# Performance work log

Hardware: AMD Instinct MI355X
Metric: run time of the kernel (lower is better)

Reference implementation:

```python
import jax, jax.numpy as jnp
import numpy as np

B, L, DIM = 4, 2048, 512
H, D = 8, 64
SCALE = D ** -0.5
NEG = -10000.0


def setup_inputs() -> dict:
    key = jax.random.key(0)
    ks = jax.random.split(key, 5)
    std = 1.0 / np.sqrt(DIM)
    return {
        "x": jax.random.normal(ks[0], (B, L, DIM), dtype=jnp.float32),
        "wq": jax.random.normal(ks[1], (H * D, DIM), dtype=jnp.float32) * std,
        "wk": jax.random.normal(ks[2], (H * D, DIM), dtype=jnp.float32) * std,
        "wv": jax.random.normal(ks[3], (H * D, DIM), dtype=jnp.float32) * std,
        "wo": jax.random.normal(ks[4], (DIM, H * D), dtype=jnp.float32) * std,
    }


def reference(x, wq, wk, wv, wo):
    b, l, _ = x.shape
    # projections (torch Linear: y = x @ W.T), split heads -> [b,h,l,d]
    q = (x @ wq.T).reshape(b, l, H, D).transpose(0, 2, 1, 3)
    k = (x @ wk.T).reshape(b, l, H, D).transpose(0, 2, 1, 3)
    v = (x @ wv.T).reshape(b, l, H, D).transpose(0, 2, 1, 3)
    scores = jnp.einsum("bhld,bhsd->bhls", q, k) * SCALE
    scores = jnp.nan_to_num(scores, nan=0.0, posinf=10000.0, neginf=NEG)
    diag = jnp.eye(l, dtype=bool)[None, None]  # [1,1,l,l]
    scores = jnp.where(diag, NEG, scores)
    attn = jax.nn.softmax(scores, axis=-1)
    attn = jnp.where(diag, 0.0, attn)
    attn = jnp.nan_to_num(attn, nan=0.0, posinf=0.0, neginf=0.0)
    out = jnp.einsum("bhls,bhsd->bhld", attn, v)
    out = out.transpose(0, 2, 1, 3).reshape(b, l, H * D)
    return out @ wo.T
```

## Files before the change

### kernel.cpp

```cpp
#include <hip/hip_runtime.h>
#include <hip/hip_bf16.h>


#define Bsz 4
#define Lsz 2048
#define DIMsz 512
#define Hsz 8
#define Dsz 64

typedef _Float16 f16;
typedef __attribute__((ext_vector_type(8))) _Float16 f16x8;
typedef __attribute__((ext_vector_type(4))) _Float16 f16x4;
typedef __attribute__((ext_vector_type(2))) __fp16 fp16x2;
typedef __attribute__((ext_vector_type(4))) float f32x4;
typedef __attribute__((ext_vector_type(16))) float f32x16;
typedef unsigned int u32;
typedef __attribute__((ext_vector_type(2))) unsigned int u32x2;

#if __has_builtin(__builtin_amdgcn_exp2f)
#define EXP2(x) __builtin_amdgcn_exp2f(x)
#else
#define EXP2(x) __expf(0.6931471805599453f * (x))
#endif

__device__ __forceinline__ u32 pack2(float a, float b) {
#if __has_builtin(__builtin_amdgcn_cvt_pkrtz)
    fp16x2 h = __builtin_amdgcn_cvt_pkrtz(a, b);
    return __builtin_bit_cast(u32, h);
#else
    fp16x2 h; h.x = (__fp16)a; h.y = (__fp16)b;
    return __builtin_bit_cast(u32, h);
#endif
}

__device__ __forceinline__ float addpair(u32 p, float c) {
#if __has_builtin(__builtin_amdgcn_fdot2)
    fp16x2 ones; ones.x = (__fp16)1.0f; ones.y = (__fp16)1.0f;
    return __builtin_amdgcn_fdot2(__builtin_bit_cast(fp16x2, p), ones, c, false);
#else
    fp16x2 h = __builtin_bit_cast(fp16x2, p);
    return c + (float)h.x + (float)h.y;
#endif
}

#if __has_builtin(__builtin_amdgcn_permlane32_swap)
__device__ __forceinline__ void plswap(u32& a, u32& b) {
    u32x2 r = __builtin_amdgcn_permlane32_swap(a, b, false, false);
    a = r.x; b = r.y;
}
#else
__device__ __forceinline__ void plswap(u32& a, u32& b) {
    u32 sa = (u32)__shfl_xor((int)a, 32);
    u32 sb = (u32)__shfl_xor((int)b, 32);
    bool hi = (threadIdx.x & 32) != 0;
    u32 na = hi ? sb : a;
    u32 nb = hi ? b : sa;
    a = na; b = nb;
}
#endif

__device__ __forceinline__ void gl2lds16(const void* g, void* l) {
    __builtin_amdgcn_global_load_lds(
        (const __attribute__((address_space(1))) u32*)g,
        (__attribute__((address_space(3))) u32*)l, 16, 0, 0);
}

__global__ __launch_bounds__(256) void pack_f16(
    const float* __restrict__ x, const float* __restrict__ wq,
    const float* __restrict__ wk, const float* __restrict__ wv,
    const float* __restrict__ wo,
    f16* __restrict__ xh, f16* __restrict__ w3h, f16* __restrict__ woh)
{
    int bx = blockIdx.x, seg, blk;
    if (bx < 4096) { seg = 0; blk = bx; }
    else { seg = 1 + ((bx - 4096) >> 8); blk = (bx - 4096) & 255; }
    const float* s; f16* d; float sc = 1.0f;
    switch (seg) {
        case 0: s = x;  d = xh;            break;
        case 1: s = wq; d = w3h;           sc = 0.18033688011112042f; break;
        case 2: s = wk; d = w3h + 262144;  break;
        case 3: s = wv; d = w3h + 524288;  break;
        default: s = wo; d = woh;          break;
    }
    int i = (blk * 256 + threadIdx.x) * 4;
    float4 v = *(const float4*)(s + i);
    f16x4 o;
    o.x = (f16)(v.x * sc); o.y = (f16)(v.y * sc);
    o.z = (f16)(v.z * sc); o.w = (f16)(v.w * sc);
    *(f16x4*)(d + i) = o;
}

__global__ __launch_bounds__(256) void gemm_qkv_f16(
    const f16* __restrict__ A, const f16* __restrict__ B,
    f16* __restrict__ qh, f16* __restrict__ kh, f16* __restrict__ vth)
{
    __shared__ __align__(16) char smem[32768];
    f16* Ash = (f16*)smem;
    f16* Bsh = (f16*)(smem + 16384);

    const int tid = threadIdx.x;
    const int w = tid >> 6, lane = tid & 63;
    const int quad = lane >> 4, low = lane & 15;
    const int wm = w >> 1, wn = w & 1;
    const int m0 = blockIdx.y * 128, n0 = blockIdx.x * 128;

    f32x4 acc[4][4];
    #pragma unroll
    for (int i = 0; i < 4; i++)
        #pragma unroll
        for (int j = 0; j < 4; j++) acc[i][j] = (f32x4){0.f, 0.f, 0.f, 0.f};

    #pragma unroll 1
    for (int k0 = 0; k0 < DIMsz; k0 += 64) {
        __syncthreads();
        #pragma unroll
        for (int j = 0; j < 4; j++) {
            int t = j * 256 + tid;
            int r = t >> 3, g = t & 7;
            int gc = (g ^ (r & 7)) * 8;
            char* lb = (char*)Ash + (j * 256 + w * 64) * 16;
            gl2lds16(A + (size_t)(m0 + r) * DIMsz + k0 + gc, lb);
            char* lb2 = (char*)Bsh + (j * 256 + w * 64) * 16;
            gl2lds16(B + (size_t)(n0 + r) * DIMsz + k0 + gc, lb2);
        }
        __syncthreads();

        #pragma unroll
        for (int ks2 = 0; ks2 < 2; ks2++) {
            f16x8 af[4], bf[4];
            #pragma unroll
            for (int mt = 0; mt < 4; mt++) {
                int ar = wm * 64 + mt * 16 + low;
                int c = ks2 * 4 + quad;
                af[mt] = *(const f16x8*)&Ash[ar * 64 + ((c ^ (ar & 7)) << 3)];
            }
            #pragma unroll
            for (int nt = 0; nt < 4; nt++) {
                int br = wn * 64 + nt * 16 + low;
                int c = ks2 * 4 + quad;
                bf[nt] = *(const f16x8*)&Bsh[br * 64 + ((c ^ (br & 7)) << 3)];
            }
            #pragma unroll
            for (int mt = 0; mt < 4; mt++)
                #pragma unroll
                for (int nt = 0; nt < 4; nt++)
                    acc[mt][nt] = __builtin_amdgcn_mfma_f32_16x16x32_f16(
                        af[mt], bf[nt], acc[mt][nt], 0, 0, 0);
        }
    }

    const int proj = n0 >> 9;
    if (proj < 2) {
        f16* dst = (proj == 0) ? qh : kh;
        #pragma unroll
        for (int nt = 0; nt < 4; nt++) {
            int n = n0 + wn * 64 + nt * 16 + low;
            int c = n & 511, h = c >> 6, d = c & 63;
            #pragma unroll
            for (int mt = 0; mt < 4; mt++)
                #pragma unroll
                for (int r = 0; r < 4; r++) {
                    int m = m0 + wm * 64 + mt * 16 + quad * 4 + r;
                    int b_ = m >> 11, l = m & (Lsz - 1);
                    size_t bh = (size_t)(b_ * Hsz + h);
                    dst[(bh * Lsz + l) * Dsz + d] = (f16)acc[mt][nt][r];
                }
        }
    } else {
        const int hb = (n0 & 511) >> 6;
        f16* Tv = (f16*)smem;
        const int b_ = m0 >> 11, l0 = m0 & (Lsz - 1);
        #pragma unroll 1
        for (int hs = 0; hs < 2; hs++) {
            __syncthreads();
            if (wn == hs) {
                #pragma unroll
                for (int nt = 0; nt < 4; nt++) {
                    int d = nt * 16 + low;
                    #pragma unroll
                    for (int mt = 0; mt < 4; mt++)
                        #pragma unroll
                        for (int r = 0; r < 4; r++) {
                            int l = wm * 64 + mt * 16 + quad * 4 + r;
                            Tv[d * 136 + l] = (f16)acc[mt][nt][r];
                        }
                }
            }
            __syncthreads();
            int d = tid >> 2, seg = tid & 3;
            size_t bh = (size_t)(b_ * Hsz + hb + hs);
            f16* dstp = vth + (bh * 64 + d) * (size_t)Lsz + l0 + seg * 32;
            const f16* srcp = Tv + d * 136 + seg * 32;
            #pragma unroll
            for (int j = 0; j < 4; j++)
                *(f16x8*)(dstp + j * 8) = *(const f16x8*)(srcp + j * 8);
        }
    }
}

__global__ __launch_bounds__(256, 2) void attn_mfma(
    const f16* __restrict__ q, const f16* __restrict__ k,
    const f16* __restrict__ vt, f16* __restrict__ ctx)
{
    __shared__ __align__(16) char smem[65536];
    __shared__ float Ls[4][2][32];

    const int tid = threadIdx.x;
    const int w = tid >> 6, lane = tid & 63;
    const int col = lane & 31;
    const int h = lane >> 5;
    const int bh = blockIdx.x;
    const int qb = blockIdx.y;
    const int q0 = qb * 64;
    const size_t kvb = (size_t)bh * Lsz;

    f16x8 qf[2][4];
    #pragma unroll
    for (int qt = 0; qt < 2; qt++)
        #pragma unroll
        for (int s = 0; s < 4; s++)
            qf[qt][s] = *(const f16x8*)(q + (kvb + q0 + qt * 32 + col) * Dsz
                                          + s * 16 + h * 8);

    const f16* kp; const f16* vp;
    {
        int rk = tid >> 3, gk = tid & 7;
        kp = k + (kvb + rk) * Dsz + ((gk ^ (rk & 7)) << 3);
        int rv = tid >> 4, gv = tid & 15;
        vp = vt + ((size_t)bh * Dsz + rv) * Lsz + ((gv ^ (rv & 15)) << 3);
    }

    char* kl[2]; char* vl[2];
    const f16* kfp[2][4];
    const f16* vfp[2][2][2];
    const int rk = w * 32 + col;
    #pragma unroll
    for (int b = 0; b < 2; b++) {
        f16* Ks = (f16*)(smem + b * 32768);
        f16* Vs = (f16*)(smem + b * 32768 + 16384);
        kl[b] = (char*)Ks + (w * 64) * 16;
        vl[b] = (char*)Vs + (w * 64) * 16;
        #pragma unroll
        for (int s = 0; s < 4; s++)
            kfp[b][s] = Ks + rk * 64 + (((s * 2 + h) ^ (rk & 7)) << 3);
        #pragma unroll
        for (int dt = 0; dt < 2; dt++)
            #pragma unroll
            for (int ks = 0; ks < 2; ks++) {
                int rv = dt * 32 + col, cv = w * 4 + ks * 2 + h;
                vfp[b][dt][ks] = Vs + rv * 128 + ((cv ^ (rv & 15)) << 3);
            }
    }

    f32x16 acc[2][2];
    #pragma unroll
    for (int qt = 0; qt < 2; qt++)
        #pragma unroll
        for (int dt = 0; dt < 2; dt++)
            #pragma unroll
            for (int i = 0; i < 16; i++) acc[qt][dt][i] = 0.f;
    float lsum[2] = {0.f, 0.f};

    const int drnd_i = qb >> 1;
    const int dqt = w - (qb & 1) * 2;

    gl2lds16(kp,        kl[0]);
    gl2lds16(kp + 2048, kl[0] + 4096);
    gl2lds16(kp + 4096, kl[0] + 8192);
    gl2lds16(kp + 6144, kl[0] + 12288);
    gl2lds16(vp,            vl[0]);
    gl2lds16(vp + 16 * Lsz, vl[0] + 4096);
    gl2lds16(vp + 32 * Lsz, vl[0] + 8192);
    gl2lds16(vp + 48 * Lsz, vl[0] + 12288);
    kp += 128 * Dsz; vp += 128;
    __syncthreads();

    int b = 0;
    #pragma unroll 1
    for (int r = 0; r < 16; r++) {
        if (r < 15) {
            char* knl = kl[b ^ 1]; char* vnl = vl[b ^ 1];
            gl2lds16(kp,        knl);
            gl2lds16(kp + 2048, knl + 4096);
            gl2lds16(kp + 4096, knl + 8192);
            gl2lds16(kp + 6144, knl + 12288);
            gl2lds16(vp,            vnl);
            gl2lds16(vp + 16 * Lsz, vnl + 4096);
            gl2lds16(vp + 32 * Lsz, vnl + 8192);
            gl2lds16(vp + 48 * Lsz, vnl + 12288);
            kp += 128 * Dsz; vp += 128;
        }

        f32x16 st[2];
        #pragma unroll
        for (int i = 0; i < 16; i++) { st[0][i] = 0.f; st[1][i] = 0.f; }
        #pragma unroll
        for (int s = 0; s < 4; s++) {
            f16x8 kf = *(const f16x8*)kfp[b][s];
            st[0] = __builtin_amdgcn_mfma_f32_32x32x16_f16(kf, qf[0][s], st[0], 0, 0, 0);
            st[1] = __builtin_amdgcn_mfma_f32_32x32x16_f16(kf, qf[1][s], st[1], 0, 0, 0);
        }

        union { u32 u[4]; f16x8 v; } pf[2][2];
        const bool drnd = (r == drnd_i);
        #pragma unroll
        for (int qt = 0; qt < 2; qt++) {
            float pv[16];
            #pragma unroll
            for (int i = 0; i < 16; i++) pv[i] = EXP2(st[qt][i]);
            if (drnd && qt == dqt) {
                #pragma unroll
                for (int i = 0; i < 16; i++) {
                    int row = (i & 3) + 8 * (i >> 2) + 4 * h;
                    pv[i] = (row == col) ? 0.f : pv[i];
                }
            }
            u32 P2[8];
            #pragma unroll
            for (int j = 0; j < 8; j++) {
                P2[j] = pack2(pv[2 * j], pv[2 * j + 1]);
                lsum[qt] = addpair(P2[j], lsum[qt]);
            }
            plswap(P2[0], P2[2]); plswap(P2[1], P2[3]);
            plswap(P2[4], P2[6]); plswap(P2[5], P2[7]);
            #pragma unroll
            for (int jj = 0; jj < 4; jj++) {
                pf[qt][0].u[jj] = P2[jj];
                pf[qt][1].u[jj] = P2[4 + jj];
            }
        }

        #pragma unroll
        for (int dt = 0; dt < 2; dt++)
            #pragma unroll
            for (int ks = 0; ks < 2; ks++) {
                f16x8 vf = *(const f16x8*)vfp[b][dt][ks];
                acc[0][dt] = __builtin_amdgcn_mfma_f32_32x32x16_f16(
                    vf, pf[0][ks].v, acc[0][dt], 0, 0, 0);
                acc[1][dt] = __builtin_amdgcn_mfma_f32_32x32x16_f16(
                    vf, pf[1][ks].v, acc[1][dt], 0, 0, 0);
            }

        __syncthreads();
        b ^= 1;
    }

    #pragma unroll
    for (int qt = 0; qt < 2; qt++) {
        lsum[qt] += __shfl_xor(lsum[qt], 32);
        if (h == 0) Ls[w][qt][col] = lsum[qt];
    }

    float* Om = (float*)smem;
    __syncthreads();
    if (w == 1 || w == 3) {
        float* og = Om + (w >> 1) * 4096;
        #pragma unroll
        for (int qt = 0; qt < 2; qt++)
            #pragma unroll
            for (int dt = 0; dt < 2; dt++)
                #pragma unroll
                for (int i = 0; i < 16; i++) {
                    int row = (i & 3) + 8 * (i >> 2) + 4 * h;
                    og[(dt * 32 + row) * 64 + qt * 32 + col] = acc[qt][dt][i];
                }
    }
    __syncthreads();
    if (w == 0 || w == 2) {
        const float* og = Om + (w >> 1) * 4096;
        #pragma unroll
        for (int qt = 0; qt < 2; qt++)
            #pragma unroll
            for (int dt = 0; dt < 2; dt++)
                #pragma unroll
                for (int i = 0; i < 16; i++) {
                    int row = (i & 3) + 8 * (i >> 2) + 4 * h;
                    acc[qt][dt][i] += og[(dt * 32 + row) * 64 + qt * 32 + col];
                }
    }
    __syncthreads();
    if (w == 2) {
        #pragma unroll
        for (int qt = 0; qt < 2; qt++)
            #pragma unroll
            for (int dt = 0; dt < 2; dt++)
                #pragma unroll
                for (int i = 0; i < 16; i++) {
                    int row = (i & 3) + 8 * (i >> 2) + 4 * h;
                    Om[(dt * 32 + row) * 64 + qt * 32 + col] = acc[qt][dt][i];
                }
    }
    __syncthreads();
    if (w == 0) {
        #pragma unroll
        for (int qt = 0; qt < 2; qt++)
            #pragma unroll
            for (int dt = 0; dt < 2; dt++)
                #pragma unroll
                for (int i = 0; i < 16; i++) {
                    int row = (i & 3) + 8 * (i >> 2) + 4 * h;
                    acc[qt][dt][i] += Om[(dt * 32 + row) * 64 + qt * 32 + col];
                }
        const int bb = bh >> 3, hh = bh & 7;
        #pragma unroll
        for (int qt = 0; qt < 2; qt++) {
            float ls = Ls[0][qt][col] + Ls[1][qt][col]
                     + Ls[2][qt][col] + Ls[3][qt][col];
            const float inv = 1.0f / ls;
            f16* op = ctx + ((size_t)(bb * Lsz + q0 + qt * 32 + col)) * DIMsz
                          + hh * 64;
            #pragma unroll
            for (int dt = 0; dt < 2; dt++)
                #pragma unroll
                for (int r4 = 0; r4 < 4; r4++) {
                    f16x4 o;
                    o.x = (f16)(acc[qt][dt][4 * r4 + 0] * inv);
                    o.y = (f16)(acc[qt][dt][4 * r4 + 1] * inv);
                    o.z = (f16)(acc[qt][dt][4 * r4 + 2] * inv);
                    o.w = (f16)(acc[qt][dt][4 * r4 + 3] * inv);
                    *(f16x4*)(op + dt * 32 + 8 * r4 + 4 * h) = o;
                }
        }
    }
}

__global__ __launch_bounds__(256) void gemm_out_f16(
    const f16* __restrict__ A, const f16* __restrict__ B,
    float* __restrict__ C)
{
    __shared__ f16 Ash[64 * 64];
    __shared__ f16 Bsh[64 * 64];
    const int tid = threadIdx.x;
    const int w = tid >> 6, lane = tid & 63;
    const int quad = lane >> 4, low = lane & 15;
    const int wm = w >> 1, wn = w & 1;
    const int m0 = blockIdx.y * 64, n0 = blockIdx.x * 64;

    f32x4 acc[2][2];
    #pragma unroll
    for (int i = 0; i < 2; i++)
        #pragma unroll
        for (int j = 0; j < 2; j++) acc[i][j] = (f32x4){0.f, 0.f, 0.f, 0.f};

    #pragma unroll 1
    for (int k0 = 0; k0 < DIMsz; k0 += 64) {
        __syncthreads();
        #pragma unroll
        for (int j = 0; j < 2; j++) {
            int t = j * 256 + tid;
            int r = t >> 3, g = t & 7;
            int gc = (g ^ (r & 7)) * 8;
            char* lb = (char*)Ash + (j * 256 + w * 64) * 16;
            gl2lds16(A + (size_t)(m0 + r) * DIMsz + k0 + gc, lb);
            char* lb2 = (char*)Bsh + (j * 256 + w * 64) * 16;
            gl2lds16(B + (size_t)(n0 + r) * DIMsz + k0 + gc, lb2);
        }
        __syncthreads();

        #pragma unroll
        for (int ks2 = 0; ks2 < 2; ks2++) {
            f16x8 af[2], bf[2];
            #pragma unroll
            for (int mt = 0; mt < 2; mt++) {
                int ar = wm * 32 + mt * 16 + low;
                int c = ks2 * 4 + quad;
                af[mt] = *(const f16x8*)&Ash[ar * 64 + ((c ^ (ar & 7)) << 3)];
            }
            #pragma unroll
            for (int nt = 0; nt < 2; nt++) {
                int br = wn * 32 + nt * 16 + low;
                int c = ks2 * 4 + quad;
                bf[nt] = *(const f16x8*)&Bsh[br * 64 + ((c ^ (br & 7)) << 3)];
            }
            #pragma unroll
            for (int mt = 0; mt < 2; mt++)
                #pragma unroll
                for (int nt = 0; nt < 2; nt++)
                    acc[mt][nt] = __builtin_amdgcn_mfma_f32_16x16x32_f16(
                        af[mt], bf[nt], acc[mt][nt], 0, 0, 0);
        }
    }

    #pragma unroll
    for (int mt = 0; mt < 2; mt++)
        #pragma unroll
        for (int r = 0; r < 4; r++) {
            int m = m0 + wm * 32 + mt * 16 + quad * 4 + r;
            #pragma unroll
            for (int nt = 0; nt < 2; nt++) {
                int n = n0 + wn * 32 + nt * 16 + low;
                C[(size_t)m * DIMsz + n] = acc[mt][nt][r];
            }
        }
}

extern "C" void kernel_launch(void* const* d_in, const int* in_sizes, int n_in,
                              void* d_out, int out_size, void* d_ws, size_t ws_size,
                              hipStream_t stream) {
    const float* x  = (const float*)d_in[0];
    const float* wq = (const float*)d_in[1];
    const float* wk = (const float*)d_in[2];
    const float* wv = (const float*)d_in[3];
    const float* wo = (const float*)d_in[4];
    float* out = (float*)d_out;

    const size_t NTOK = (size_t)Bsz * Lsz;
    const size_t XSZ  = NTOK * DIMsz;

    f16* xh   = (f16*)d_ws;
    f16* w3h  = xh + XSZ;
    f16* woh  = w3h + 3 * 262144;
    f16* qh   = woh + 262144;
    f16* kh   = qh + XSZ;
    f16* vth  = kh + XSZ;
    f16* ctxh = vth + XSZ;

    pack_f16<<<5120, 256, 0, stream>>>(x, wq, wk, wv, wo, xh, w3h, woh);

    dim3 g1(1536 / 128, NTOK / 128);
    gemm_qkv_f16<<<g1, 256, 0, stream>>>(xh, w3h, qh, kh, vth);

    dim3 g2(Bsz * Hsz, Lsz / 64);
    attn_mfma<<<g2, 256, 0, stream>>>(qh, kh, vth, ctxh);

    dim3 g3(DIMsz / 64, NTOK / 64);
    gemm_out_f16<<<g3, 256, 0, stream>>>(ctxh, woh, out);
}
```

Measured before the change: 172.3 us.

## Load K fragments directly from global in attention; widen output GEMM K-tile

The attention kernel stops staging K tiles through LDS. Each wave now reads its K fragments straight from global memory into registers every round. This halves the shared-memory footprint so launch bounds can request four blocks per CU instead of two, trading LDS reuse for more occupancy and more global or L2 traffic. Separately, the output projection GEMM doubles its K tile from 64 to 128, with the swizzle and load loops adjusted, to halve the number of barrier-separated load phases.

```diff
diff --git a/kernel.cpp b/kernel.cpp
--- a/kernel.cpp
+++ b/kernel.cpp
@@ -198,11 +198,11 @@
     }
 }
 
-__global__ __launch_bounds__(256, 2) void attn_mfma(
+__global__ __launch_bounds__(256, 4) void attn_mfma(
     const f16* __restrict__ q, const f16* __restrict__ k,
     const f16* __restrict__ vt, f16* __restrict__ ctx)
 {
-    __shared__ __align__(16) char smem[65536];
+    __shared__ __align__(16) char smem[32768];
     __shared__ float Ls[4][2][32];
 
     const int tid = threadIdx.x;
@@ -222,27 +222,20 @@
             qf[qt][s] = *(const f16x8*)(q + (kvb + q0 + qt * 32 + col) * Dsz
                                           + s * 16 + h * 8);
 
-    const f16* kp; const f16* vp;
+    const f16* kgp = k + (kvb + w * 32 + col) * Dsz + h * 8;
+
+    const f16* vp;
     {
-        int rk = tid >> 3, gk = tid & 7;
-        kp = k + (kvb + rk) * Dsz + ((gk ^ (rk & 7)) << 3);
         int rv = tid >> 4, gv = tid & 15;
         vp = vt + ((size_t)bh * Dsz + rv) * Lsz + ((gv ^ (rv & 15)) << 3);
     }
 
-    char* kl[2]; char* vl[2];
-    const f16* kfp[2][4];
+    char* vl[2];
     const f16* vfp[2][2][2];
-    const int rk = w * 32 + col;
     #pragma unroll
     for (int b = 0; b < 2; b++) {
-        f16* Ks = (f16*)(smem + b * 32768);
-        f16* Vs = (f16*)(smem + b * 32768 + 16384);
-        kl[b] = (char*)Ks + (w * 64) * 16;
+        f16* Vs = (f16*)(smem + b * 16384);
         vl[b] = (char*)Vs + (w * 64) * 16;
-        #pragma unroll
-        for (int s = 0; s < 4; s++)
-            kfp[b][s] = Ks + rk * 64 + (((s * 2 + h) ^ (rk & 7)) << 3);
         #pragma unroll
         for (int dt = 0; dt < 2; dt++)
             #pragma unroll
@@ -264,31 +257,29 @@
     const int drnd_i = qb >> 1;
     const int dqt = w - (qb & 1) * 2;
 
-    gl2lds16(kp,        kl[0]);
-    gl2lds16(kp + 2048, kl[0] + 4096);
-    gl2lds16(kp + 4096, kl[0] + 8192);
-    gl2lds16(kp + 6144, kl[0] + 12288);
     gl2lds16(vp,            vl[0]);
     gl2lds16(vp + 16 * Lsz, vl[0] + 4096);
     gl2lds16(vp + 32 * Lsz, vl[0] + 8192);
     gl2lds16(vp + 48 * Lsz, vl[0] + 12288);
-    kp += 128 * Dsz; vp += 128;
+    vp += 128;
     __syncthreads();
 
     int b = 0;
     #pragma unroll 1
     for (int r = 0; r < 16; r++) {
+        f16x8 kf[4];
+        #pragma unroll
+        for (int s = 0; s < 4; s++)
+            kf[s] = *(const f16x8*)(kgp + s * 16);
+        kgp += 128 * Dsz;
+
         if (r < 15) {
-            char* knl = kl[b ^ 1]; char* vnl = vl[b ^ 1];
-            gl2lds16(kp,        knl);
-            gl2lds16(kp + 2048, knl + 4096);
-            gl2lds16(kp + 4096, knl + 8192);
-            gl2lds16(kp + 6144, knl + 12288);
+            char* vnl = vl[b ^ 1];
             gl2lds16(vp,            vnl);
             gl2lds16(vp + 16 * Lsz, vnl + 4096);
             gl2lds16(vp + 32 * Lsz, vnl + 8192);
             gl2lds16(vp + 48 * Lsz, vnl + 12288);
-            kp += 128 * Dsz; vp += 128;
+            vp += 128;
         }
 
         f32x16 st[2];
@@ -296,9 +287,8 @@
         for (int i = 0; i < 16; i++) { st[0][i] = 0.f; st[1][i] = 0.f; }
         #pragma unroll
         for (int s = 0; s < 4; s++) {
-            f16x8 kf = *(const f16x8*)kfp[b][s];
-            st[0] = __builtin_amdgcn_mfma_f32_32x32x16_f16(kf, qf[0][s], st[0], 0, 0, 0);
-            st[1] = __builtin_amdgcn_mfma_f32_32x32x16_f16(kf, qf[1][s], st[1], 0, 0, 0);
+            st[0] = __builtin_amdgcn_mfma_f32_32x32x16_f16(kf[s], qf[0][s], st[0], 0, 0, 0);
+            st[1] = __builtin_amdgcn_mfma_f32_32x32x16_f16(kf[s], qf[1][s], st[1], 0, 0, 0);
         }
 
         union { u32 u[4]; f16x8 v; } pf[2][2];
@@ -428,8 +418,8 @@
     const f16* __restrict__ A, const f16* __restrict__ B,
     float* __restrict__ C)
 {
-    __shared__ f16 Ash[64 * 64];
-    __shared__ f16 Bsh[64 * 64];
+    __shared__ f16 Ash[64 * 128];
+    __shared__ f16 Bsh[64 * 128];
     const int tid = threadIdx.x;
     const int w = tid >> 6, lane = tid & 63;
     const int quad = lane >> 4, low = lane & 15;
@@ -443,13 +433,13 @@
         for (int j = 0; j < 2; j++) acc[i][j] = (f32x4){0.f, 0.f, 0.f, 0.f};
 
     #pragma unroll 1
-    for (int k0 = 0; k0 < DIMsz; k0 += 64) {
+    for (int k0 = 0; k0 < DIMsz; k0 += 128) {
         __syncthreads();
         #pragma unroll
-        for (int j = 0; j < 2; j++) {
+        for (int j = 0; j < 4; j++) {
             int t = j * 256 + tid;
-            int r = t >> 3, g = t & 7;
-            int gc = (g ^ (r & 7)) * 8;
+            int r = t >> 4, g = t & 15;
+            int gc = (g ^ (r & 15)) * 8;
             char* lb = (char*)Ash + (j * 256 + w * 64) * 16;
             gl2lds16(A + (size_t)(m0 + r) * DIMsz + k0 + gc, lb);
             char* lb2 = (char*)Bsh + (j * 256 + w * 64) * 16;
@@ -458,19 +448,19 @@
         __syncthreads();
 
         #pragma unroll
-        for (int ks2 = 0; ks2 < 2; ks2++) {
+        for (int ks2 = 0; ks2 < 4; ks2++) {
             f16x8 af[2], bf[2];
             #pragma unroll
             for (int mt = 0; mt < 2; mt++) {
                 int ar = wm * 32 + mt * 16 + low;
                 int c = ks2 * 4 + quad;
-                af[mt] = *(const f16x8*)&Ash[ar * 64 + ((c ^ (ar & 7)) << 3)];
+                af[mt] = *(const f16x8*)&Ash[ar * 128 + ((c ^ (ar & 15)) << 3)];
             }
             #pragma unroll
             for (int nt = 0; nt < 2; nt++) {
                 int br = wn * 32 + nt * 16 + low;
                 int c = ks2 * 4 + quad;
-                bf[nt] = *(const f16x8*)&Bsh[br * 64 + ((c ^ (br & 7)) << 3)];
+                bf[nt] = *(const f16x8*)&Bsh[br * 128 + ((c ^ (br & 15)) << 3)];
             }
             #pragma unroll
             for (int mt = 0; mt < 2; mt++)
```

Measured after the change: 313.3 us. 1.82x slower.
